# Optimization experiments

Measured on AMD Instinct MI355X. Metric: run time of the kernel, lower is better.

## Reference

```python
import jax, jax.numpy as jnp
import numpy as np

N, E = 50000, 800000
D_IN, D_HID, D_OUT = 128, 64, 32
NEG_SLOPE = 0.2


def _gat_layer(h_in, src, dst, W, a_s, a_d, b):
    # h_in: [N, din], W: [din, dout]
    h = h_in @ W                                   # [N, dout]
    alpha_src = h @ a_s                            # [N]
    alpha_dst = h @ a_d                            # [N]
    e = jax.nn.leaky_relu(alpha_src[src] + alpha_dst[dst], NEG_SLOPE)  # [E']
    # segment softmax over incoming edges of each dst node
    m = jax.ops.segment_max(e, dst, num_segments=N)
    ex = jnp.exp(e - m[dst])
    s = jax.ops.segment_sum(ex, dst, num_segments=N)
    w = ex / s[dst]                                # [E']
    out = jax.ops.segment_sum(h[src] * w[:, None], dst, num_segments=N)
    return out + b


def setup_inputs() -> dict:
    key = jax.random.key(0)
    ks = jax.random.split(key, 16)
    x = jax.random.normal(ks[0], (N, D_IN), dtype=jnp.float32)
    edge_index = jax.random.randint(ks[1], (2, E), 0, N, dtype=jnp.int64)
    dims = [(D_IN, D_HID), (D_HID, D_HID), (D_HID, D_OUT)]
    inp = {"x": x, "edge_index": edge_index}
    for i, (din, dout) in enumerate(dims):
        sc = 1.0 / np.sqrt(din)
        inp[f"W{i}"] = jax.random.normal(ks[2 + 4 * i], (din, dout), dtype=jnp.float32) * sc
        inp[f"as{i}"] = jax.random.normal(ks[3 + 4 * i], (dout,), dtype=jnp.float32) * 0.1
        inp[f"ad{i}"] = jax.random.normal(ks[4 + 4 * i], (dout,), dtype=jnp.float32) * 0.1
        inp[f"b{i}"] = jnp.zeros((dout,), dtype=jnp.float32)
    return inp


def reference(x, edge_index, W0, as0, ad0, b0, W1, as1, ad1, b1, W2, as2, ad2, b2):
    # add self loops (PyG GATConv default)
    loop = jnp.arange(N, dtype=edge_index.dtype)
    src = jnp.concatenate([edge_index[0], loop])
    dst = jnp.concatenate([edge_index[1], loop])
    h = jax.nn.relu(_gat_layer(x, src, dst, W0, as0, ad0, b0))
    h = jax.nn.relu(_gat_layer(h, src, dst, W1, as1, ad1, b1))
    h = jnp.tanh(_gat_layer(h, src, dst, W2, as2, ad2, b2))
    return h
```

## Files before the change

### kernel.cpp

```cpp
#include <hip/hip_runtime.h>
#include <hip/hip_fp16.h>
#include <math.h>

#define N_NODES 50000
#define E_EDGES 800000
#define ETOT    (E_EDGES + N_NODES)

#define BUCK_SHIFT 9
#define BUCK_SZ   (1 << BUCK_SHIFT)
#define NBUCK ((N_NODES + BUCK_SZ - 1) >> BUCK_SHIFT)
#define BS_EPT 16
#define BS_THREADS 256
#define BS_EPB (BS_THREADS * BS_EPT)
#define BS_NBLK ((ETOT + BS_EPB - 1) / BS_EPB)

#define GEMM0_GRID ((N_NODES + 63) / 64)
#define HPB ((ETOT + GEMM0_GRID - 1) / GEMM0_GRID)

__global__ __launch_bounds__(256)
void gemm0_hist_kernel(const float* __restrict__ X, const float* __restrict__ W,
                       const float* __restrict__ a_s, const float* __restrict__ a_d,
                       const int* __restrict__ ei, int* __restrict__ bcnt,
                       __half* __restrict__ H16, float* __restrict__ asrc,
                       float* __restrict__ adst)
{
    constexpr int DIN = 128, DOUT = 64;
    constexpr int COLG = DOUT / 4;
    constexpr int BM   = 64;

    __shared__ float Wl[DIN * DOUT];
    __shared__ int   lh[NBUCK];

    const int tid = threadIdx.x;
    const int row0b = blockIdx.x * BM;

    for (int i = tid; i < DIN * DOUT / 4; i += 256)
        ((float4*)Wl)[i] = ((const float4*)W)[i];
    __syncthreads();

    const int tx = tid % COLG;
    const int ty = tid / COLG;
    const int r0 = ty * 4;
    const int c0 = tx * 4;

    const float* Xr[4];
#pragma unroll
    for (int i = 0; i < 4; ++i) {
        int gr = row0b + r0 + i;
        Xr[i] = X + (size_t)min(gr, N_NODES - 1) * DIN;
    }

    float acc[4][4] = {};
#pragma unroll 4
    for (int kk = 0; kk < DIN; kk += 4) {
        float a[4][4], w[4][4];
#pragma unroll
        for (int i = 0; i < 4; ++i)
            *(float4*)a[i] = *(const float4*)&Xr[i][kk];
#pragma unroll
        for (int j = 0; j < 4; ++j)
            *(float4*)w[j] = *(const float4*)&Wl[(kk + j) * DOUT + c0];
#pragma unroll
        for (int i = 0; i < 4; ++i)
#pragma unroll
            for (int j = 0; j < 4; ++j)
                acc[i][j] = fmaf(a[i][0], w[0][j],
                            fmaf(a[i][1], w[1][j],
                            fmaf(a[i][2], w[2][j],
                            fmaf(a[i][3], w[3][j], acc[i][j]))));
    }

    float as4[4], ad4[4];
    *(float4*)as4 = *(const float4*)&a_s[c0];
    *(float4*)ad4 = *(const float4*)&a_d[c0];

#pragma unroll
    for (int i = 0; i < 4; ++i) {
        const int gr = row0b + r0 + i;
        float ps = acc[i][0] * as4[0] + acc[i][1] * as4[1] +
                   acc[i][2] * as4[2] + acc[i][3] * as4[3];
        float pd = acc[i][0] * ad4[0] + acc[i][1] * ad4[1] +
                   acc[i][2] * ad4[2] + acc[i][3] * ad4[3];
#pragma unroll
        for (int off = COLG / 2; off >= 1; off >>= 1) {
            ps += __shfl_xor(ps, off, 64);
            pd += __shfl_xor(pd, off, 64);
        }
        if (gr < N_NODES) {
            __half2 p01 = __floats2half2_rn(acc[i][0], acc[i][1]);
            __half2 p23 = __floats2half2_rn(acc[i][2], acc[i][3]);
            uint2 pk;
            pk.x = *(unsigned int*)&p01;
            pk.y = *(unsigned int*)&p23;
            *(uint2*)&H16[gr * DOUT + c0] = pk;
            if (tx == 0) { asrc[gr] = ps; adst[gr] = pd; }
        }
    }

    for (int i = tid; i < NBUCK; i += 256) lh[i] = 0;
    __syncthreads();
    const int h0 = blockIdx.x * HPB;
    const int hend = min(h0 + HPB, ETOT);
    for (int eid = h0 + tid; eid < hend; eid += 256) {
        int dst = (eid < E_EDGES) ? ei[E_EDGES + eid] : (eid - E_EDGES);
        atomicAdd(&lh[dst >> BUCK_SHIFT], 1);
    }
    __syncthreads();
    for (int i = tid; i < NBUCK; i += 256)
        if (lh[i] > 0) atomicAdd(&bcnt[i], lh[i]);
}

template<int DIN, int DOUT>
__global__ __launch_bounds__(256)
void gemm_alpha_kernel(const float* __restrict__ X, const float* __restrict__ W,
                       const float* __restrict__ a_s, const float* __restrict__ a_d,
                       __half* __restrict__ H16, float* __restrict__ asrc,
                       float* __restrict__ adst)
{
    constexpr int COLG = DOUT / 4;
    constexpr int ROWG = 256 / COLG;
    constexpr int BM   = ROWG * 4;

    __shared__ float Wl[DIN * DOUT];

    const int tid = threadIdx.x;
    const int row0b = blockIdx.x * BM;

    for (int i = tid; i < DIN * DOUT / 4; i += 256)
        ((float4*)Wl)[i] = ((const float4*)W)[i];
    __syncthreads();

    const int tx = tid % COLG;
    const int ty = tid / COLG;
    const int r0 = ty * 4;
    const int c0 = tx * 4;

    const float* Xr[4];
#pragma unroll
    for (int i = 0; i < 4; ++i) {
        int gr = row0b + r0 + i;
        Xr[i] = X + (size_t)min(gr, N_NODES - 1) * DIN;
    }

    float acc[4][4] = {};
#pragma unroll 4
    for (int kk = 0; kk < DIN; kk += 4) {
        float a[4][4], w[4][4];
#pragma unroll
        for (int i = 0; i < 4; ++i)
            *(float4*)a[i] = *(const float4*)&Xr[i][kk];
#pragma unroll
        for (int j = 0; j < 4; ++j)
            *(float4*)w[j] = *(const float4*)&Wl[(kk + j) * DOUT + c0];
#pragma unroll
        for (int i = 0; i < 4; ++i)
#pragma unroll
            for (int j = 0; j < 4; ++j)
                acc[i][j] = fmaf(a[i][0], w[0][j],
                            fmaf(a[i][1], w[1][j],
                            fmaf(a[i][2], w[2][j],
                            fmaf(a[i][3], w[3][j], acc[i][j]))));
    }

    float as4[4], ad4[4];
    *(float4*)as4 = *(const float4*)&a_s[c0];
    *(float4*)ad4 = *(const float4*)&a_d[c0];

#pragma unroll
    for (int i = 0; i < 4; ++i) {
        const int gr = row0b + r0 + i;
        float ps = acc[i][0] * as4[0] + acc[i][1] * as4[1] +
                   acc[i][2] * as4[2] + acc[i][3] * as4[3];
        float pd = acc[i][0] * ad4[0] + acc[i][1] * ad4[1] +
                   acc[i][2] * ad4[2] + acc[i][3] * ad4[3];
#pragma unroll
        for (int off = COLG / 2; off >= 1; off >>= 1) {
            ps += __shfl_xor(ps, off, 64);
            pd += __shfl_xor(pd, off, 64);
        }
        if (gr < N_NODES) {
            __half2 p01 = __floats2half2_rn(acc[i][0], acc[i][1]);
            __half2 p23 = __floats2half2_rn(acc[i][2], acc[i][3]);
            uint2 pk;
            pk.x = *(unsigned int*)&p01;
            pk.y = *(unsigned int*)&p23;
            *(uint2*)&H16[gr * DOUT + c0] = pk;
            if (tx == 0) { asrc[gr] = ps; adst[gr] = pd; }
        }
    }
}

__global__ __launch_bounds__(BS_THREADS)
void binscatter_kernel(const int* __restrict__ ei, const int* __restrict__ bcnt,
                       int* __restrict__ cur, unsigned int* __restrict__ tmp)
{
    __shared__ int lcnt[NBUCK];
    __shared__ int lbase[NBUCK];
    __shared__ int lscan[128];
    const int t = threadIdx.x;

    if (t < 128) {
        const int v = (t < NBUCK) ? bcnt[t] : 0;
        lscan[t] = v;
        __syncthreads();
        for (int off = 1; off < 128; off <<= 1) {
            int u = (t >= off) ? lscan[t - off] : 0;
            __syncthreads();
            lscan[t] += u;
            __syncthreads();
        }
        if (t < NBUCK) lbase[t] = lscan[t] - v;
    } else {
        __syncthreads();
        for (int off = 1; off < 128; off <<= 1) { __syncthreads(); __syncthreads(); }
    }
    for (int i = t; i < NBUCK; i += BS_THREADS) lcnt[i] = 0;
    __syncthreads();

    const int e0 = blockIdx.x * BS_EPB;
    unsigned int pk[BS_EPT];
    int rk[BS_EPT];
    int bk[BS_EPT];
#pragma unroll
    for (int k = 0; k < BS_EPT; ++k) {
        const int eid = e0 + k * BS_THREADS + t;
        bk[k] = -1;
        if (eid < ETOT) {
            int src, dst;
            if (eid < E_EDGES) { src = ei[eid]; dst = ei[E_EDGES + eid]; }
            else               { src = dst = eid - E_EDGES; }
            bk[k] = dst >> BUCK_SHIFT;
            pk[k] = ((unsigned int)dst << 16) | (unsigned int)src;
            rk[k] = atomicAdd(&lcnt[bk[k]], 1);
        }
    }
    __syncthreads();
    for (int i = t; i < NBUCK; i += BS_THREADS)
        if (lcnt[i] > 0) lbase[i] += atomicAdd(&cur[i], lcnt[i]);
    __syncthreads();
#pragma unroll
    for (int k = 0; k < BS_EPT; ++k)
        if (bk[k] >= 0) tmp[lbase[bk[k]] + rk[k]] = pk[k];
}

__global__ __launch_bounds__(BUCK_SZ)
void bucket_sort_kernel(const unsigned int* __restrict__ tmp,
                        const int* __restrict__ bcnt,
                        unsigned int* __restrict__ csr_pk,
                        int* __restrict__ offs)
{
    __shared__ int lcnt[BUCK_SZ];
    __shared__ int loff[BUCK_SZ];
    __shared__ int lcur[BUCK_SZ];
    __shared__ int sbase;
    const int bk = blockIdx.x;
    const int t  = threadIdx.x;

    {
        const int v = (t < NBUCK) ? bcnt[t] : 0;
        lcnt[t] = v;
        __syncthreads();
        for (int off = 1; off < 128; off <<= 1) {
            int u = (t >= off && t < 128) ? lcnt[t - off] : 0;
            __syncthreads();
            if (t < 128) lcnt[t] += u;
            __syncthreads();
        }
        if (t == bk) sbase = lcnt[t] - v;
    }
    __syncthreads();
    const int base = sbase;
    const int cnt  = bcnt[bk];

    lcnt[t] = 0;
    __syncthreads();
    for (int i = t; i < cnt; i += BUCK_SZ)
        atomicAdd(&lcnt[(tmp[base + i] >> 16) & (BUCK_SZ - 1)], 1);
    __syncthreads();

    const int v = lcnt[t];
    loff[t] = v;
    __syncthreads();
    for (int off = 1; off < BUCK_SZ; off <<= 1) {
        int u = (t >= off) ? loff[t - off] : 0;
        __syncthreads();
        loff[t] += u;
        __syncthreads();
    }
    const int excl = loff[t] - v;

    const int g = (bk << BUCK_SHIFT) + t;
    if (g <= N_NODES) offs[g] = base + excl;

    lcur[t] = excl;
    __syncthreads();
    for (int i = t; i < cnt; i += BUCK_SZ) {
        const unsigned int pk = tmp[base + i];
        const int l = (pk >> 16) & (BUCK_SZ - 1);
        const int pos = atomicAdd(&lcur[l], 1);
        csr_pk[base + pos] = pk;
    }
}

template<int DOUT, int ACT>
__global__ __launch_bounds__(256)
void node_agg_kernel(const int* __restrict__ offs,
                     const unsigned int* __restrict__ csr_pk,
                     const float* __restrict__ asrc,
                     const float* __restrict__ adst,
                     const __half* __restrict__ H16,
                     const float* __restrict__ b,
                     float* __restrict__ out)
{
    constexpr int FL    = DOUT / 8;
    constexpr int SLOTS = 64 / FL;
    const int wv   = threadIdx.x >> 6;
    const int lane = threadIdx.x & 63;
    const int fl   = lane % FL;
    const int slot = lane / FL;
    const int node = blockIdx.x * 4 + wv;
    if (node >= N_NODES) return;

    const int beg = offs[node];
    const int end = offs[node + 1];
    const float adn = adst[node];
    const __half* __restrict__ Hf = H16 + fl * 8;

    float s = 0.f;
    float acc[8] = {};

    int eid = beg + slot;
    bool valid = (eid < end);
    unsigned int pk = valid ? csr_pk[eid] : 0u;

    for (int cb = beg; cb < end; cb += SLOTS) {
        const int nid = cb + SLOTS + slot;
        const bool nvalid = (nid < end);
        const unsigned int npk = nvalid ? csr_pk[nid] : 0u;

        float p = 0.f;
        uint4 h = make_uint4(0u, 0u, 0u, 0u);
        if (valid) {
            const unsigned int src = pk & 0xffffu;
            float v = asrc[src] + adn;
            v = fmaxf(v, 0.2f * v);
            p = __expf(fminf(v, 80.f));
            h = *(const uint4*)(Hf + src * DOUT);
        }
        const float2 f0 = __half22float2(*(const __half2*)&h.x);
        const float2 f1 = __half22float2(*(const __half2*)&h.y);
        const float2 f2 = __half22float2(*(const __half2*)&h.z);
        const float2 f3 = __half22float2(*(const __half2*)&h.w);
        s += p;
        acc[0] = fmaf(p, f0.x, acc[0]);
        acc[1] = fmaf(p, f0.y, acc[1]);
        acc[2] = fmaf(p, f1.x, acc[2]);
        acc[3] = fmaf(p, f1.y, acc[3]);
        acc[4] = fmaf(p, f2.x, acc[4]);
        acc[5] = fmaf(p, f2.y, acc[5]);
        acc[6] = fmaf(p, f3.x, acc[6]);
        acc[7] = fmaf(p, f3.y, acc[7]);
        valid = nvalid;
        pk = npk;
    }

#pragma unroll
    for (int off = FL; off < 64; off <<= 1) {
        s += __shfl_xor(s, off, 64);
#pragma unroll
        for (int j = 0; j < 8; ++j)
            acc[j] += __shfl_xor(acc[j], off, 64);
    }

    if (slot == 0) {
        const float inv = 1.f / s;
        float o[8];
#pragma unroll
        for (int j = 0; j < 8; ++j) {
            float v = acc[j] * inv + b[fl * 8 + j];
            o[j] = (ACT == 0) ? fmaxf(v, 0.f) : tanhf(v);
        }
        *(float4*)&out[node * DOUT + fl * 8]     = *(float4*)&o[0];
        *(float4*)&out[node * DOUT + fl * 8 + 4] = *(float4*)&o[4];
    }
}


extern "C" void kernel_launch(void* const* d_in, const int* in_sizes, int n_in,
                              void* d_out, int out_size, void* d_ws, size_t ws_size,
                              hipStream_t stream)
{
    const float* x  = (const float*)d_in[0];
    const int*   ei = (const int*)d_in[1];
    const float* W0 = (const float*)d_in[2];
    const float* as0= (const float*)d_in[3];
    const float* ad0= (const float*)d_in[4];
    const float* b0 = (const float*)d_in[5];
    const float* W1 = (const float*)d_in[6];
    const float* as1= (const float*)d_in[7];
    const float* ad1= (const float*)d_in[8];
    const float* b1 = (const float*)d_in[9];
    const float* W2 = (const float*)d_in[10];
    const float* as2= (const float*)d_in[11];
    const float* ad2= (const float*)d_in[12];
    const float* b2 = (const float*)d_in[13];
    float* out = (float*)d_out;

    char* wsb = (char*)d_ws;
    auto take = [&](size_t bytes) {
        char* p = wsb;
        wsb += (bytes + 255) & ~size_t(255);
        return p;
    };
    __half* h16    = (__half*)take(sizeof(__half) * N_NODES * 64);
    float* buf_act = (float*)take(sizeof(float) * N_NODES * 64);
    float* asrc    = (float*)take(sizeof(float) * N_NODES);
    float* adst    = (float*)take(sizeof(float) * N_NODES);
    int*   offs    = (int*)take(sizeof(int) * (N_NODES + 1));
    int*   bc      = (int*)take(sizeof(int) * NBUCK * 2);
    int*   bcnt    = bc;
    int*   cur     = bc + NBUCK;
    unsigned int* tmp    = (unsigned int*)take(sizeof(unsigned int) * ETOT);
    unsigned int* csr_pk = (unsigned int*)take(sizeof(unsigned int) * ETOT);

    hipMemsetAsync(bc, 0, sizeof(int) * NBUCK * 2, stream);

    gemm0_hist_kernel<<<GEMM0_GRID, 256, 0, stream>>>(
        x, W0, as0, ad0, ei, bcnt, h16, asrc, adst);

    binscatter_kernel<<<BS_NBLK, BS_THREADS, 0, stream>>>(ei, bcnt, cur, tmp);
    bucket_sort_kernel<<<NBUCK, BUCK_SZ, 0, stream>>>(tmp, bcnt, csr_pk, offs);

    const int agg_grid = (N_NODES + 3) / 4;
    node_agg_kernel<64, 0><<<agg_grid, 256, 0, stream>>>(
        offs, csr_pk, asrc, adst, h16, b0, buf_act);

    gemm_alpha_kernel<64, 64><<<GEMM0_GRID, 256, 0, stream>>>(
        buf_act, W1, as1, ad1, h16, asrc, adst);
    node_agg_kernel<64, 0><<<agg_grid, 256, 0, stream>>>(
        offs, csr_pk, asrc, adst, h16, b1, buf_act);

    gemm_alpha_kernel<64, 32><<<(N_NODES + 127) / 128, 256, 0, stream>>>(
        buf_act, W2, as2, ad2, h16, asrc, adst);
    node_agg_kernel<32, 1><<<agg_grid, 256, 0, stream>>>(
        offs, csr_pk, asrc, adst, h16, b2, out);
}
```

Measured before the change: 187.7 us.

## Split histogram out and co-schedule layer-0 GEMM with edge binscatter

Edge-bucket counting moves out of the layer-0 GEMM into its own small histogram kernel. The GEMM and the binscatter pass then run as one launch, with blocks split by blockIdx between the two jobs. The aim is to let the memory-bound scatter overlap the compute-bound GEMM and to drop a serial launch. The cost is an extra histogram pass that rereads the dst indices, and scatter blocks reserve the GEMM's shared memory size, which may reduce their occupancy.

```diff
diff --git a/kernel.cpp b/kernel.cpp
--- a/kernel.cpp
+++ b/kernel.cpp
@@ -15,21 +15,227 @@
 #define BS_NBLK ((ETOT + BS_EPB - 1) / BS_EPB)
 
 #define GEMM0_GRID ((N_NODES + 63) / 64)
-#define HPB ((ETOT + GEMM0_GRID - 1) / GEMM0_GRID)
+#define PACK_GRID (GEMM0_GRID + BS_NBLK)
+
+__global__ __launch_bounds__(BS_THREADS)
+void hist_kernel(const int* __restrict__ ei, int* __restrict__ bcnt)
+{
+    __shared__ int lcnt[NBUCK];
+    const int t = threadIdx.x;
+    for (int i = t; i < NBUCK; i += BS_THREADS) lcnt[i] = 0;
+    __syncthreads();
+    const int e0 = blockIdx.x * BS_EPB;
+#pragma unroll
+    for (int k = 0; k < BS_EPT; ++k) {
+        const int eid = e0 + k * BS_THREADS + t;
+        if (eid < ETOT) {
+            int dst = (eid < E_EDGES) ? ei[E_EDGES + eid] : (eid - E_EDGES);
+            atomicAdd(&lcnt[dst >> BUCK_SHIFT], 1);
+        }
+    }
+    __syncthreads();
+    for (int i = t; i < NBUCK; i += BS_THREADS)
+        if (lcnt[i] > 0) atomicAdd(&bcnt[i], lcnt[i]);
+}
 
 __global__ __launch_bounds__(256)
-void gemm0_hist_kernel(const float* __restrict__ X, const float* __restrict__ W,
+void gemm0_binscatter_kernel(const float* __restrict__ X,
+                             const float* __restrict__ W,
+                             const float* __restrict__ a_s,
+                             const float* __restrict__ a_d,
+                             __half* __restrict__ H16,
+                             float* __restrict__ asrc,
+                             float* __restrict__ adst,
+                             const int* __restrict__ ei,
+                             const int* __restrict__ bcnt,
+                             int* __restrict__ cur,
+                             unsigned int* __restrict__ tmp)
+{
+    __shared__ float smem[128 * 64];
+    const int t = threadIdx.x;
+
+    if (blockIdx.x < GEMM0_GRID) {
+        constexpr int DIN = 128, DOUT = 64, COLG = 16;
+        float* Wl = smem;
+        for (int i = t; i < DIN * DOUT / 4; i += 256)
+            ((float4*)Wl)[i] = ((const float4*)W)[i];
+        __syncthreads();
+
+        const int row0b = blockIdx.x * 64;
+        const int tx = t % COLG;
+        const int ty = t / COLG;
+        const int r0 = ty * 4;
+        const int c0 = tx * 4;
+
+        const float* Xr[4];
+#pragma unroll
+        for (int i = 0; i < 4; ++i) {
+            int gr = row0b + r0 + i;
+            Xr[i] = X + (size_t)min(gr, N_NODES - 1) * DIN;
+        }
+
+        float acc[4][4] = {};
+#pragma unroll 4
+        for (int kk = 0; kk < DIN; kk += 4) {
+            float a[4][4], w[4][4];
+#pragma unroll
+            for (int i = 0; i < 4; ++i)
+                *(float4*)a[i] = *(const float4*)&Xr[i][kk];
+#pragma unroll
+            for (int j = 0; j < 4; ++j)
+                *(float4*)w[j] = *(const float4*)&Wl[(kk + j) * DOUT + c0];
+#pragma unroll
+            for (int i = 0; i < 4; ++i)
+#pragma unroll
+                for (int j = 0; j < 4; ++j)
+                    acc[i][j] = fmaf(a[i][0], w[0][j],
+                                fmaf(a[i][1], w[1][j],
+                                fmaf(a[i][2], w[2][j],
+                                fmaf(a[i][3], w[3][j], acc[i][j]))));
+        }
+
+        float as4[4], ad4[4];
+        *(float4*)as4 = *(const float4*)&a_s[c0];
+        *(float4*)ad4 = *(const float4*)&a_d[c0];
+
+#pragma unroll
+        for (int i = 0; i < 4; ++i) {
+            const int gr = row0b + r0 + i;
+            float ps = acc[i][0] * as4[0] + acc[i][1] * as4[1] +
+                       acc[i][2] * as4[2] + acc[i][3] * as4[3];
+            float pd = acc[i][0] * ad4[0] + acc[i][1] * ad4[1] +
+                       acc[i][2] * ad4[2] + acc[i][3] * ad4[3];
+#pragma unroll
+            for (int off = COLG / 2; off >= 1; off >>= 1) {
+                ps += __shfl_xor(ps, off, 64);
+                pd += __shfl_xor(pd, off, 64);
+            }
+            if (gr < N_NODES) {
+                __half2 p01 = __floats2half2_rn(acc[i][0], acc[i][1]);
+                __half2 p23 = __floats2half2_rn(acc[i][2], acc[i][3]);
+                uint2 pk;
+                pk.x = *(unsigned int*)&p01;
+                pk.y = *(unsigned int*)&p23;
+                *(uint2*)&H16[gr * DOUT + c0] = pk;
+                if (tx == 0) { asrc[gr] = ps; adst[gr] = pd; }
+            }
+        }
+    } else {
+        int* lcnt  = (int*)smem;
+        int* lbase = lcnt + 128;
+        int* lscan = lbase + 128;
+
+        const int v = (t < NBUCK) ? bcnt[t] : 0;
+        lscan[t] = v;
+        __syncthreads();
+        for (int off = 1; off < 256; off <<= 1) {
+            int u = (t >= off) ? lscan[t - off] : 0;
+            __syncthreads();
+            lscan[t] += u;
+            __syncthreads();
+        }
+        if (t < NBUCK) lbase[t] = lscan[t] - v;
+        for (int i = t; i < NBUCK; i += 256) lcnt[i] = 0;
+        __syncthreads();
+
+        const int e0 = (blockIdx.x - GEMM0_GRID) * BS_EPB;
+        unsigned int pk[BS_EPT];
+        int rk[BS_EPT];
+        int bk[BS_EPT];
+#pragma unroll
+        for (int k = 0; k < BS_EPT; ++k) {
+            const int eid = e0 + k * BS_THREADS + t;
+            bk[k] = -1;
+            if (eid < ETOT) {
+                int src, dst;
+                if (eid < E_EDGES) { src = ei[eid]; dst = ei[E_EDGES + eid]; }
+                else               { src = dst = eid - E_EDGES; }
+                bk[k] = dst >> BUCK_SHIFT;
+                pk[k] = ((unsigned int)dst << 16) | (unsigned int)src;
+                rk[k] = atomicAdd(&lcnt[bk[k]], 1);
+            }
+        }
+        __syncthreads();
+        for (int i = t; i < NBUCK; i += 256)
+            if (lcnt[i] > 0) lbase[i] += atomicAdd(&cur[i], lcnt[i]);
+        __syncthreads();
+#pragma unroll
+        for (int k = 0; k < BS_EPT; ++k)
+            if (bk[k] >= 0) tmp[lbase[bk[k]] + rk[k]] = pk[k];
+    }
+}
+
+__global__ __launch_bounds__(BUCK_SZ)
+void bucket_sort_kernel(const unsigned int* __restrict__ tmp,
+                        const int* __restrict__ bcnt,
+                        unsigned int* __restrict__ csr_pk,
+                        int* __restrict__ offs)
+{
+    __shared__ int lcnt[BUCK_SZ];
+    __shared__ int loff[BUCK_SZ];
+    __shared__ int lcur[BUCK_SZ];
+    __shared__ int sbase;
+    const int bk = blockIdx.x;
+    const int t  = threadIdx.x;
+
+    {
+        const int v = (t < NBUCK) ? bcnt[t] : 0;
+        lcnt[t] = v;
+        __syncthreads();
+        for (int off = 1; off < 128; off <<= 1) {
+            int u = (t >= off && t < 128) ? lcnt[t - off] : 0;
+            __syncthreads();
+            if (t < 128) lcnt[t] += u;
+            __syncthreads();
+        }
+        if (t == bk) sbase = lcnt[t] - v;
+    }
+    __syncthreads();
+    const int base = sbase;
+    const int cnt  = bcnt[bk];
+
+    lcnt[t] = 0;
+    __syncthreads();
+    for (int i = t; i < cnt; i += BUCK_SZ)
+        atomicAdd(&lcnt[(tmp[base + i] >> 16) & (BUCK_SZ - 1)], 1);
+    __syncthreads();
+
+    const int v = lcnt[t];
+    loff[t] = v;
+    __syncthreads();
+    for (int off = 1; off < BUCK_SZ; off <<= 1) {
+        int u = (t >= off) ? loff[t - off] : 0;
+        __syncthreads();
+        loff[t] += u;
+        __syncthreads();
+    }
+    const int excl = loff[t] - v;
+
+    const int g = (bk << BUCK_SHIFT) + t;
+    if (g <= N_NODES) offs[g] = base + excl;
+
+    lcur[t] = excl;
+    __syncthreads();
+    for (int i = t; i < cnt; i += BUCK_SZ) {
+        const unsigned int pk = tmp[base + i];
+        const int l = (pk >> 16) & (BUCK_SZ - 1);
+        const int pos = atomicAdd(&lcur[l], 1);
+        csr_pk[base + pos] = pk;
+    }
+}
+
+template<int DIN, int DOUT>
+__global__ __launch_bounds__(256)
+void gemm_alpha_kernel(const float* __restrict__ X, const float* __restrict__ W,
                        const float* __restrict__ a_s, const float* __restrict__ a_d,
-                       const int* __restrict__ ei, int* __restrict__ bcnt,
                        __half* __restrict__ H16, float* __restrict__ asrc,
                        float* __restrict__ adst)
 {
-    constexpr int DIN = 128, DOUT = 64;
     constexpr int COLG = DOUT / 4;
-    constexpr int BM   = 64;
+    constexpr int ROWG = 256 / COLG;
+    constexpr int BM   = ROWG * 4;
 
     __shared__ float Wl[DIN * DOUT];
-    __shared__ int   lh[NBUCK];
 
     const int tid = threadIdx.x;
     const int row0b = blockIdx.x * BM;
@@ -95,210 +301,6 @@
             *(uint2*)&H16[gr * DOUT + c0] = pk;
             if (tx == 0) { asrc[gr] = ps; adst[gr] = pd; }
         }
-    }
-
-    for (int i = tid; i < NBUCK; i += 256) lh[i] = 0;
-    __syncthreads();
-    const int h0 = blockIdx.x * HPB;
-    const int hend = min(h0 + HPB, ETOT);
-    for (int eid = h0 + tid; eid < hend; eid += 256) {
-        int dst = (eid < E_EDGES) ? ei[E_EDGES + eid] : (eid - E_EDGES);
-        atomicAdd(&lh[dst >> BUCK_SHIFT], 1);
-    }
-    __syncthreads();
-    for (int i = tid; i < NBUCK; i += 256)
-        if (lh[i] > 0) atomicAdd(&bcnt[i], lh[i]);
-}
-
-template<int DIN, int DOUT>
-__global__ __launch_bounds__(256)
-void gemm_alpha_kernel(const float* __restrict__ X, const float* __restrict__ W,
-                       const float* __restrict__ a_s, const float* __restrict__ a_d,
-                       __half* __restrict__ H16, float* __restrict__ asrc,
-                       float* __restrict__ adst)
-{
-    constexpr int COLG = DOUT / 4;
-    constexpr int ROWG = 256 / COLG;
-    constexpr int BM   = ROWG * 4;
-
-    __shared__ float Wl[DIN * DOUT];
-
-    const int tid = threadIdx.x;
-    const int row0b = blockIdx.x * BM;
-
-    for (int i = tid; i < DIN * DOUT / 4; i += 256)
-        ((float4*)Wl)[i] = ((const float4*)W)[i];
-    __syncthreads();
-
-    const int tx = tid % COLG;
-    const int ty = tid / COLG;
-    const int r0 = ty * 4;
-    const int c0 = tx * 4;
-
-    const float* Xr[4];
-#pragma unroll
-    for (int i = 0; i < 4; ++i) {
-        int gr = row0b + r0 + i;
-        Xr[i] = X + (size_t)min(gr, N_NODES - 1) * DIN;
-    }
-
-    float acc[4][4] = {};
-#pragma unroll 4
-    for (int kk = 0; kk < DIN; kk += 4) {
-        float a[4][4], w[4][4];
-#pragma unroll
-        for (int i = 0; i < 4; ++i)
-            *(float4*)a[i] = *(const float4*)&Xr[i][kk];
-#pragma unroll
-        for (int j = 0; j < 4; ++j)
-            *(float4*)w[j] = *(const float4*)&Wl[(kk + j) * DOUT + c0];
-#pragma unroll
-        for (int i = 0; i < 4; ++i)
-#pragma unroll
-            for (int j = 0; j < 4; ++j)
-                acc[i][j] = fmaf(a[i][0], w[0][j],
-                            fmaf(a[i][1], w[1][j],
-                            fmaf(a[i][2], w[2][j],
-                            fmaf(a[i][3], w[3][j], acc[i][j]))));
-    }
-
-    float as4[4], ad4[4];
-    *(float4*)as4 = *(const float4*)&a_s[c0];
-    *(float4*)ad4 = *(const float4*)&a_d[c0];
-
-#pragma unroll
-    for (int i = 0; i < 4; ++i) {
-        const int gr = row0b + r0 + i;
-        float ps = acc[i][0] * as4[0] + acc[i][1] * as4[1] +
-                   acc[i][2] * as4[2] + acc[i][3] * as4[3];
-        float pd = acc[i][0] * ad4[0] + acc[i][1] * ad4[1] +
-                   acc[i][2] * ad4[2] + acc[i][3] * ad4[3];
-#pragma unroll
-        for (int off = COLG / 2; off >= 1; off >>= 1) {
-            ps += __shfl_xor(ps, off, 64);
-            pd += __shfl_xor(pd, off, 64);
-        }
-        if (gr < N_NODES) {
-            __half2 p01 = __floats2half2_rn(acc[i][0], acc[i][1]);
-            __half2 p23 = __floats2half2_rn(acc[i][2], acc[i][3]);
-            uint2 pk;
-            pk.x = *(unsigned int*)&p01;
-            pk.y = *(unsigned int*)&p23;
-            *(uint2*)&H16[gr * DOUT + c0] = pk;
-            if (tx == 0) { asrc[gr] = ps; adst[gr] = pd; }
-        }
-    }
-}
-
-__global__ __launch_bounds__(BS_THREADS)
-void binscatter_kernel(const int* __restrict__ ei, const int* __restrict__ bcnt,
-                       int* __restrict__ cur, unsigned int* __restrict__ tmp)
-{
-    __shared__ int lcnt[NBUCK];
-    __shared__ int lbase[NBUCK];
-    __shared__ int lscan[128];
-    const int t = threadIdx.x;
-
-    if (t < 128) {
-        const int v = (t < NBUCK) ? bcnt[t] : 0;
-        lscan[t] = v;
-        __syncthreads();
-        for (int off = 1; off < 128; off <<= 1) {
-            int u = (t >= off) ? lscan[t - off] : 0;
-            __syncthreads();
-            lscan[t] += u;
-            __syncthreads();
-        }
-        if (t < NBUCK) lbase[t] = lscan[t] - v;
-    } else {
-        __syncthreads();
-        for (int off = 1; off < 128; off <<= 1) { __syncthreads(); __syncthreads(); }
-    }
-    for (int i = t; i < NBUCK; i += BS_THREADS) lcnt[i] = 0;
-    __syncthreads();
-
-    const int e0 = blockIdx.x * BS_EPB;
-    unsigned int pk[BS_EPT];
-    int rk[BS_EPT];
-    int bk[BS_EPT];
-#pragma unroll
-    for (int k = 0; k < BS_EPT; ++k) {
-        const int eid = e0 + k * BS_THREADS + t;
-        bk[k] = -1;
-        if (eid < ETOT) {
-            int src, dst;
-            if (eid < E_EDGES) { src = ei[eid]; dst = ei[E_EDGES + eid]; }
-            else               { src = dst = eid - E_EDGES; }
-            bk[k] = dst >> BUCK_SHIFT;
-            pk[k] = ((unsigned int)dst << 16) | (unsigned int)src;
-            rk[k] = atomicAdd(&lcnt[bk[k]], 1);
-        }
-    }
-    __syncthreads();
-    for (int i = t; i < NBUCK; i += BS_THREADS)
-        if (lcnt[i] > 0) lbase[i] += atomicAdd(&cur[i], lcnt[i]);
-    __syncthreads();
-#pragma unroll
-    for (int k = 0; k < BS_EPT; ++k)
-        if (bk[k] >= 0) tmp[lbase[bk[k]] + rk[k]] = pk[k];
-}
-
-__global__ __launch_bounds__(BUCK_SZ)
-void bucket_sort_kernel(const unsigned int* __restrict__ tmp,
-                        const int* __restrict__ bcnt,
-                        unsigned int* __restrict__ csr_pk,
-                        int* __restrict__ offs)
-{
-    __shared__ int lcnt[BUCK_SZ];
-    __shared__ int loff[BUCK_SZ];
-    __shared__ int lcur[BUCK_SZ];
-    __shared__ int sbase;
-    const int bk = blockIdx.x;
-    const int t  = threadIdx.x;
-
-    {
-        const int v = (t < NBUCK) ? bcnt[t] : 0;
-        lcnt[t] = v;
-        __syncthreads();
-        for (int off = 1; off < 128; off <<= 1) {
-            int u = (t >= off && t < 128) ? lcnt[t - off] : 0;
-            __syncthreads();
-            if (t < 128) lcnt[t] += u;
-            __syncthreads();
-        }
-        if (t == bk) sbase = lcnt[t] - v;
-    }
-    __syncthreads();
-    const int base = sbase;
-    const int cnt  = bcnt[bk];
-
-    lcnt[t] = 0;
-    __syncthreads();
-    for (int i = t; i < cnt; i += BUCK_SZ)
-        atomicAdd(&lcnt[(tmp[base + i] >> 16) & (BUCK_SZ - 1)], 1);
-    __syncthreads();
-
-    const int v = lcnt[t];
-    loff[t] = v;
-    __syncthreads();
-    for (int off = 1; off < BUCK_SZ; off <<= 1) {
-        int u = (t >= off) ? loff[t - off] : 0;
-        __syncthreads();
-        loff[t] += u;
-        __syncthreads();
-    }
-    const int excl = loff[t] - v;
-
-    const int g = (bk << BUCK_SHIFT) + t;
-    if (g <= N_NODES) offs[g] = base + excl;
-
-    lcur[t] = excl;
-    __syncthreads();
-    for (int i = t; i < cnt; i += BUCK_SZ) {
-        const unsigned int pk = tmp[base + i];
-        const int l = (pk >> 16) & (BUCK_SZ - 1);
-        const int pos = atomicAdd(&lcur[l], 1);
-        csr_pk[base + pos] = pk;
     }
 }
 
@@ -425,10 +427,11 @@
 
     hipMemsetAsync(bc, 0, sizeof(int) * NBUCK * 2, stream);
 
-    gemm0_hist_kernel<<<GEMM0_GRID, 256, 0, stream>>>(
-        x, W0, as0, ad0, ei, bcnt, h16, asrc, adst);
-
-    binscatter_kernel<<<BS_NBLK, BS_THREADS, 0, stream>>>(ei, bcnt, cur, tmp);
+    hist_kernel<<<BS_NBLK, BS_THREADS, 0, stream>>>(ei, bcnt);
+
+    gemm0_binscatter_kernel<<<PACK_GRID, 256, 0, stream>>>(
+        x, W0, as0, ad0, h16, asrc, adst, ei, bcnt, cur, tmp);
+
     bucket_sort_kernel<<<NBUCK, BUCK_SZ, 0, stream>>>(tmp, bcnt, csr_pk, offs);
 
     const int agg_grid = (N_NODES + 3) / 4;
```

Measured after the change: 172.5 us. 8.1% less time.
